# Optimization experiments

Measured on AMD Instinct MI355X. Metric: run time of the kernel, lower is better.

## Reference

```python
import jax, jax.numpy as jnp
import numpy as np

B, S, D, F, E = 8, 2048, 1024, 4096, 5

def setup_inputs() -> dict:
    key = jax.random.key(0)
    ks = jax.random.split(key, 9)
    sc = 0.02
    return {
        "hidden_states": jax.random.normal(ks[0], (B, S, D), jnp.float32),
        "type_label": jax.random.randint(ks[1], (B,), 0, E, jnp.int32),
        "wi": jax.random.normal(ks[2], (E, D, F), jnp.float32) * sc,   # routed experts wi
        "wo": jax.random.normal(ks[3], (E, F, D), jnp.float32) * sc,   # routed experts wo
        "swi": jax.random.normal(ks[4], (2, D, F), jnp.float32) * sc,  # shared experts wi
        "swo": jax.random.normal(ks[5], (2, F, D), jnp.float32) * sc,  # shared experts wo
        "g1": jax.random.normal(ks[6], (3 * D, D), jnp.float32) * sc,  # gate layer 1
        "g2": jax.random.normal(ks[7], (D, 3), jnp.float32) * sc,      # gate layer 2
    }

def _dense(x, wi_, wo_):
    # T5DenseActDense with relu act, dropout=0 (eval)
    return jax.nn.relu(x @ wi_) @ wo_

def reference(hidden_states, type_label, wi, wo, swi, swo, g1, g2):
    x = hidden_states
    s0 = _dense(x, swi[0], swo[0])  # [B,S,D] shared expert 0
    s1 = _dense(x, swi[1], swo[1])  # [B,S,D] shared expert 1
    # per-sample routed expert: gather weights by label, batched GEMM
    wi_sel = wi[type_label]         # [B,D,F]
    wo_sel = wo[type_label]         # [B,F,D]
    h = jax.nn.relu(jnp.einsum('bsd,bdf->bsf', x, wi_sel))
    eo = jnp.einsum('bsf,bfd->bsd', h, wo_sel)  # [B,S,D]
    # gate on token 0 of each stream, all gates share parameters
    gate_in = jnp.concatenate([eo[:, 0], s0[:, 0], s1[:, 0]], axis=-1)  # [B,3D]
    w = jax.nn.softmax(jax.nn.relu(gate_in @ g1) @ g2, axis=-1)         # [B,3]
    w = w[:, :, None, None]
    return eo * w[:, 0] + s0 * w[:, 1] + s1 * w[:, 2]
```

## Files before the change

kernel.cpp:

```cpp
#include <hip/hip_runtime.h>
#include <hip/hip_bf16.h>
#include <cstdint>

#define B_ 8
#define S_ 2048
#define D_ 1024
#define F_ 4096
#define E_ 5

typedef __attribute__((ext_vector_type(4))) int      i32x4;
typedef __attribute__((ext_vector_type(4))) float    f32x4;
typedef __attribute__((ext_vector_type(4))) uint16_t u16x4;
typedef __attribute__((ext_vector_type(8))) uint16_t u16x8;

__device__ __forceinline__ float b2f(uint16_t u){
  union { uint32_t i; float f; } v; v.i = ((uint32_t)u) << 16; return v.f;
}
__device__ __forceinline__ uint16_t f2b(float f){
  union { float f; uint32_t i; } v; v.f = f;
  uint32_t x = v.i;
  uint32_t r = (x + 0x7FFFu + ((x >> 16) & 1u)) >> 16;
  return (uint16_t)r;
}
__device__ __forceinline__ void gload16B(const uint16_t* g, uint16_t* l){
  __builtin_amdgcn_global_load_lds(
      (const __attribute__((address_space(1))) void*)g,
      (__attribute__((address_space(3))) void*)l, 16, 0, 0);
}

__global__ __launch_bounds__(256) void cvt_bf16(
    const float* __restrict__ src, uint16_t* __restrict__ dst, long n)
{
  long i = ((long)blockIdx.x * 256 + threadIdx.x) * 8;
  const long stride = (long)gridDim.x * 256 * 8;
  for (; i + 8 <= n; i += stride){
    f32x4 a = *(const f32x4*)(src + i);
    f32x4 b = *(const f32x4*)(src + i + 4);
    u16x8 r;
#pragma unroll
    for (int k = 0; k < 4; ++k){ r[k] = f2b(a[k]); r[4 + k] = f2b(b[k]); }
    *(u16x8*)(dst + i) = r;
  }
}

__global__ __launch_bounds__(256) void transpose64(
    const float* __restrict__ src, uint16_t* __restrict__ dst, int R, int C)
{
  __shared__ uint16_t t[64][68];
  const size_t base = (size_t)blockIdx.z * R * C;
  const int r0 = blockIdx.x * 64, c0 = blockIdx.y * 64;
  const int tr = threadIdx.x >> 4;
  const int tc = (threadIdx.x & 15) * 4;
#pragma unroll
  for (int i = 0; i < 4; ++i){
    const int row = tr + i * 16;
    f32x4 v = *(const f32x4*)(src + base + (size_t)(r0 + row) * C + (c0 + tc));
    t[row][tc + 0] = f2b(v[0]); t[row][tc + 1] = f2b(v[1]);
    t[row][tc + 2] = f2b(v[2]); t[row][tc + 3] = f2b(v[3]);
  }
  __syncthreads();
#pragma unroll
  for (int i = 0; i < 4; ++i){
    const int orow = tr + i * 16;
    u16x4 v;
    v[0] = t[tc + 0][orow]; v[1] = t[tc + 1][orow];
    v[2] = t[tc + 2][orow]; v[3] = t[tc + 3][orow];
    *(u16x4*)(dst + base + (size_t)(c0 + orow) * R + (r0 + tc)) = v;
  }
}

__global__ __launch_bounds__(256) void transpose_f32(
    const float* __restrict__ src, float* __restrict__ dst, int R, int C)
{
  __shared__ float t[64][65];
  const int r0 = blockIdx.x * 64, c0 = blockIdx.y * 64;
  const int tr = threadIdx.x >> 4;
  const int tc = (threadIdx.x & 15) * 4;
#pragma unroll
  for (int i = 0; i < 4; ++i){
    const int row = tr + i * 16;
    f32x4 v = *(const f32x4*)(src + (size_t)(r0 + row) * C + (c0 + tc));
    t[row][tc + 0] = v[0]; t[row][tc + 1] = v[1];
    t[row][tc + 2] = v[2]; t[row][tc + 3] = v[3];
  }
  __syncthreads();
#pragma unroll
  for (int i = 0; i < 4; ++i){
    const int orow = tr + i * 16;
    f32x4 v;
    v[0] = t[tc + 0][orow]; v[1] = t[tc + 1][orow];
    v[2] = t[tc + 2][orow]; v[3] = t[tc + 3][orow];
    *(f32x4*)(dst + (size_t)(c0 + orow) * R + (r0 + tc)) = v;
  }
}

__global__ __launch_bounds__(256) void gate_h(
    const uint16_t* __restrict__ xb, const uint16_t* __restrict__ wiT,
    const uint16_t* __restrict__ swiT, const int* __restrict__ label,
    float* __restrict__ hbuf)
{
  const int f = blockIdx.x * 256 + threadIdx.x;
  const int path = blockIdx.y, b = blockIdx.z;
  const uint16_t* wrow = (path == 0)
      ? wiT  + ((size_t)label[b] * F_ + f) * D_
      : swiT + ((size_t)(path - 1) * F_ + f) * D_;
  __shared__ uint16_t xs[D_];
  const uint16_t* xr = xb + (size_t)b * S_ * D_;
  *(u16x4*)(xs + threadIdx.x * 4) = *(const u16x4*)(xr + threadIdx.x * 4);
  __syncthreads();
  float acc = 0.f;
  for (int d = 0; d < D_; d += 8){
    u16x8 w = *(const u16x8*)(wrow + d);
    u16x8 xv = *(const u16x8*)(xs + d);
#pragma unroll
    for (int k = 0; k < 8; ++k) acc += b2f(xv[k]) * b2f(w[k]);
  }
  hbuf[(size_t)(b * 3 + path) * F_ + f] = fmaxf(acc, 0.f);
}

__global__ __launch_bounds__(256) void gate_row(
    const uint16_t* __restrict__ woT, const uint16_t* __restrict__ swoT,
    const int* __restrict__ label, const float* __restrict__ hbuf,
    float* __restrict__ gin)
{
  const int d = blockIdx.x * 256 + threadIdx.x;
  const int path = blockIdx.y, b = blockIdx.z;
  const uint16_t* wrow = (path == 0)
      ? woT  + ((size_t)label[b] * D_ + d) * F_
      : swoT + ((size_t)(path - 1) * D_ + d) * F_;
  __shared__ float hs[F_];
  const float* hb = hbuf + (size_t)(b * 3 + path) * F_;
  for (int i = threadIdx.x; i < F_; i += 256) hs[i] = hb[i];
  __syncthreads();
  float acc = 0.f;
  for (int f = 0; f < F_; f += 8){
    u16x8 w = *(const u16x8*)(wrow + f);
    f32x4 h0 = *(const f32x4*)(hs + f);
    f32x4 h1 = *(const f32x4*)(hs + f + 4);
    acc += h0[0]*b2f(w[0]) + h0[1]*b2f(w[1]) + h0[2]*b2f(w[2]) + h0[3]*b2f(w[3])
         + h1[0]*b2f(w[4]) + h1[1]*b2f(w[5]) + h1[2]*b2f(w[6]) + h1[3]*b2f(w[7]);
  }
  gin[(size_t)(b * 3 + path) * D_ + d] = acc;
}

__global__ __launch_bounds__(256) void gate_w1(
    const float* __restrict__ gin, const float* __restrict__ g1T,
    float* __restrict__ ts)
{
  const int j = blockIdx.x * 256 + threadIdx.x;
  const int b = blockIdx.y;
  __shared__ float gs[3 * D_];
  const float* g = gin + (size_t)b * 3 * D_;
  for (int i = threadIdx.x; i < 3 * D_; i += 256) gs[i] = g[i];
  __syncthreads();
  const float* grow = g1T + (size_t)j * (3 * D_);
  float acc = 0.f;
  for (int i = 0; i < 3 * D_; i += 4){
    f32x4 w = *(const f32x4*)(grow + i);
    f32x4 gv = *(const f32x4*)(gs + i);
    acc += gv[0]*w[0] + gv[1]*w[1] + gv[2]*w[2] + gv[3]*w[3];
  }
  ts[(size_t)b * D_ + j] = fmaxf(acc, 0.f);
}

__global__ __launch_bounds__(256) void gate_w2(
    const float* __restrict__ ts, const float* __restrict__ g2,
    float* __restrict__ wgate)
{
  const int b = blockIdx.x;
  __shared__ float p0[256], p1[256], p2[256];
  const float* t = ts + (size_t)b * D_;
  float s0 = 0.f, s1 = 0.f, s2 = 0.f;
  const int j0 = threadIdx.x * 4;
#pragma unroll
  for (int jj = 0; jj < 4; ++jj){
    const float tv = t[j0 + jj];
    s0 += tv * g2[(j0 + jj) * 3 + 0];
    s1 += tv * g2[(j0 + jj) * 3 + 1];
    s2 += tv * g2[(j0 + jj) * 3 + 2];
  }
  p0[threadIdx.x] = s0; p1[threadIdx.x] = s1; p2[threadIdx.x] = s2;
  __syncthreads();
  for (int st = 128; st > 0; st >>= 1){
    if (threadIdx.x < st){
      p0[threadIdx.x] += p0[threadIdx.x + st];
      p1[threadIdx.x] += p1[threadIdx.x + st];
      p2[threadIdx.x] += p2[threadIdx.x + st];
    }
    __syncthreads();
  }
  if (threadIdx.x == 0){
    const float a = p0[0], c = p1[0], d = p2[0];
    const float m = fmaxf(a, fmaxf(c, d));
    const float e0 = expf(a - m), e1 = expf(c - m), e2 = expf(d - m);
    const float inv = 1.f / (e0 + e1 + e2);
    wgate[b * 3 + 0] = e0 * inv;
    wgate[b * 3 + 1] = e1 * inv;
    wgate[b * 3 + 2] = e2 * inv;
  }
}

template<int MODE>
__global__ __launch_bounds__(256) void gemm_bt(
    const uint16_t* __restrict__ Abase, size_t a_stride, int lda, int K,
    const uint16_t* __restrict__ Wexp, const uint16_t* __restrict__ Wsh,
    int path, int b0, const int* __restrict__ label,
    const float* __restrict__ wgate,
    void* __restrict__ Obase_, size_t o_stride, int ldo)
{
  __shared__ uint16_t As[128 * 64];
  __shared__ uint16_t Bs[128 * 64];

  const int z  = blockIdx.z;
  const int b  = b0 + z;
  const int m0 = blockIdx.x * 128;
  const int n0 = blockIdx.y * 128;

  const uint16_t* A = Abase + (size_t)z * a_stride;
  const size_t wstride = (size_t)D_ * F_;
  const uint16_t* BT = (path == 0) ? Wexp + (size_t)label[b] * wstride
                                   : Wsh  + (size_t)(path - 1) * wstride;

  const int tid  = threadIdx.x;
  const int wave = tid >> 6;
  const int lane = tid & 63;

  const uint16_t* gA = A  + (size_t)(m0 + wave * 8 + (lane >> 3)) * lda + (lane & 7) * 8;
  const uint16_t* gB = BT + (size_t)(n0 + wave * 8 + (lane >> 3)) * K   + (lane & 7) * 8;
  uint16_t* lA = As + wave * 512;
  uint16_t* lB = Bs + wave * 512;

  f32x4 acc[4][4];
#pragma unroll
  for (int i = 0; i < 4; ++i)
#pragma unroll
    for (int j = 0; j < 4; ++j) acc[i][j] = (f32x4)0.0f;

  const uint16_t* pa = As + ((wave >> 1) * 64 + (lane & 15)) * 64 + (lane >> 4) * 8;
  const uint16_t* pb = Bs + ((wave &  1) * 64 + (lane & 15)) * 64 + (lane >> 4) * 8;

  const int KT = K >> 6;
  for (int kt = 0; kt < KT; ++kt){
    __syncthreads();
#pragma unroll
    for (int q = 0; q < 4; ++q){
      gload16B(gA + (size_t)q * 32 * lda, lA + q * 2048);
      gload16B(gB + (size_t)q * 32 * K,   lB + q * 2048);
    }
    gA += 64; gB += 64;
    __syncthreads();
#pragma unroll
    for (int ks = 0; ks < 2; ++ks){
      i32x4 af[4], bf[4];
#pragma unroll
      for (int i = 0; i < 4; ++i) af[i] = *(const i32x4*)(pa + i * 1024 + ks * 32);
#pragma unroll
      for (int j = 0; j < 4; ++j) bf[j] = *(const i32x4*)(pb + j * 1024 + ks * 32);
#pragma unroll
      for (int i = 0; i < 4; ++i)
#pragma unroll
        for (int j = 0; j < 4; ++j)
          asm("v_mfma_f32_16x16x32_bf16 %0, %1, %2, %0"
              : "+v"(acc[i][j]) : "v"(af[i]), "v"(bf[j]));
    }
  }

  asm volatile("s_nop 7\n\ts_nop 7" ::);

  const int orow0 = m0 + (wave >> 1) * 64 + (lane >> 4) * 4;
  const int ocol0 = n0 + (wave &  1) * 64 + (lane & 15);

  if constexpr (MODE == 0){
    uint16_t* O = (uint16_t*)Obase_ + (size_t)z * o_stride;
#pragma unroll
    for (int i = 0; i < 4; ++i)
#pragma unroll
      for (int j = 0; j < 4; ++j){
        const int col = ocol0 + j * 16;
#pragma unroll
        for (int r = 0; r < 4; ++r){
          const int row = orow0 + i * 16 + r;
          const float v = acc[i][j][r];
          O[(size_t)row * ldo + col] = f2b(v > 0.f ? v : 0.f);
        }
      }
  } else {
    float* O = (float*)Obase_ + (size_t)z * o_stride;
    const float scale = wgate[b * 3 + path];
#pragma unroll
    for (int i = 0; i < 4; ++i)
#pragma unroll
      for (int j = 0; j < 4; ++j){
        const int col = ocol0 + j * 16;
#pragma unroll
        for (int r = 0; r < 4; ++r){
          const int row = orow0 + i * 16 + r;
          const size_t idx = (size_t)row * ldo + col;
          float v = scale * acc[i][j][r];
          if constexpr (MODE == 2) v += O[idx];
          O[idx] = v;
        }
      }
  }
}

extern "C" void kernel_launch(void* const* d_in, const int* in_sizes, int n_in,
                              void* d_out, int out_size, void* d_ws, size_t ws_size,
                              hipStream_t stream)
{
  (void)in_sizes; (void)n_in; (void)out_size;
  const float* x    = (const float*)d_in[0];
  const int*   label= (const int*)d_in[1];
  const float* wi   = (const float*)d_in[2];
  const float* wo   = (const float*)d_in[3];
  const float* swi  = (const float*)d_in[4];
  const float* swo  = (const float*)d_in[5];
  const float* g1   = (const float*)d_in[6];
  const float* g2   = (const float*)d_in[7];
  float* out = (float*)d_out;

  char* ws = (char*)d_ws;
  float* wgate = (float*)ws;
  float* gin   = (float*)(ws + 256);
  float* hbuf  = (float*)(ws + 98560);
  float* ts    = (float*)(ws + 491776);
  float* g1T   = (float*)(ws + (1u << 20));
  uint16_t* xb = (uint16_t*)(ws + (16u << 20));
  size_t off = (size_t)(16u << 20) + (size_t)B_ * S_ * D_ * 2;
  uint16_t* wiT  = (uint16_t*)(ws + off); off += (size_t)E_ * D_ * F_ * 2;
  uint16_t* swiT = (uint16_t*)(ws + off); off += (size_t)2  * D_ * F_ * 2;
  uint16_t* woT  = (uint16_t*)(ws + off); off += (size_t)E_ * D_ * F_ * 2;
  uint16_t* swoT = (uint16_t*)(ws + off); off += (size_t)2  * D_ * F_ * 2;
  uint16_t* H    = (uint16_t*)(ws + off);
  const size_t hbytes = (size_t)S_ * F_ * 2;
  const size_t hcap = (ws_size > off) ? (ws_size - off) / hbytes : 0;
  const int nb = hcap >= 8 ? 8 : hcap >= 4 ? 4 : hcap >= 2 ? 2 : 1;

  cvt_bf16<<<dim3(2048), 256, 0, stream>>>(x, xb, (long)B_ * S_ * D_);
  transpose64<<<dim3(D_/64, F_/64, E_), 256, 0, stream>>>(wi,  wiT,  D_, F_);
  transpose64<<<dim3(D_/64, F_/64, 2 ), 256, 0, stream>>>(swi, swiT, D_, F_);
  transpose64<<<dim3(F_/64, D_/64, E_), 256, 0, stream>>>(wo,  woT,  F_, D_);
  transpose64<<<dim3(F_/64, D_/64, 2 ), 256, 0, stream>>>(swo, swoT, F_, D_);
  transpose_f32<<<dim3(3*D_/64, D_/64), 256, 0, stream>>>(g1, g1T, 3*D_, D_);

  gate_h  <<<dim3(F_/256, 3, B_), 256, 0, stream>>>(xb, wiT, swiT, label, hbuf);
  gate_row<<<dim3(D_/256, 3, B_), 256, 0, stream>>>(woT, swoT, label, hbuf, gin);
  gate_w1 <<<dim3(D_/256, B_),    256, 0, stream>>>(gin, g1T, ts);
  gate_w2 <<<dim3(B_),            256, 0, stream>>>(ts, g2, wgate);

  const size_t SD = (size_t)S_ * D_;
  const size_t SF = (size_t)S_ * F_;
  for (int path = 0; path < 3; ++path){
    for (int b0 = 0; b0 < B_; b0 += nb){
      const int nbc = (b0 + nb <= B_) ? nb : (B_ - b0);
      gemm_bt<0><<<dim3(S_/128, F_/128, nbc), 256, 0, stream>>>(
          xb + (size_t)b0 * SD, SD, D_, D_, wiT, swiT, path, b0, label,
          (const float*)nullptr, H, SF, F_);
      if (path == 0)
        gemm_bt<1><<<dim3(S_/128, D_/128, nbc), 256, 0, stream>>>(
            H, SF, F_, F_, woT, swoT, path, b0, label, wgate,
            out + (size_t)b0 * SD, SD, D_);
      else
        gemm_bt<2><<<dim3(S_/128, D_/128, nbc), 256, 0, stream>>>(
            H, SF, F_, F_, woT, swoT, path, b0, label, wgate,
            out + (size_t)b0 * SD, SD, D_);
    }
  }
}
```

Measured before the change: 1.272 ms.

## Double-buffer LDS tiles to prefetch next K-tile during MFMA compute

```diff
diff --git a/kernel.cpp b/kernel.cpp
--- a/kernel.cpp
+++ b/kernel.cpp
@@ -208,8 +208,8 @@
     const float* __restrict__ wgate,
     void* __restrict__ Obase_, size_t o_stride, int ldo)
 {
-  __shared__ uint16_t As[128 * 64];
-  __shared__ uint16_t Bs[128 * 64];
+  __shared__ uint16_t As[2][128 * 64];
+  __shared__ uint16_t Bs[2][128 * 64];
 
   const int z  = blockIdx.z;
   const int b  = b0 + z;
@@ -227,8 +227,6 @@
 
   const uint16_t* gA = A  + (size_t)(m0 + wave * 8 + (lane >> 3)) * lda + (lane & 7) * 8;
   const uint16_t* gB = BT + (size_t)(n0 + wave * 8 + (lane >> 3)) * K   + (lane & 7) * 8;
-  uint16_t* lA = As + wave * 512;
-  uint16_t* lB = Bs + wave * 512;
 
   f32x4 acc[4][4];
 #pragma unroll
@@ -236,19 +234,33 @@
 #pragma unroll
     for (int j = 0; j < 4; ++j) acc[i][j] = (f32x4)0.0f;
 
-  const uint16_t* pa = As + ((wave >> 1) * 64 + (lane & 15)) * 64 + (lane >> 4) * 8;
-  const uint16_t* pb = Bs + ((wave &  1) * 64 + (lane & 15)) * 64 + (lane >> 4) * 8;
+  const int fa = ((wave >> 1) * 64 + (lane & 15)) * 64 + (lane >> 4) * 8;
+  const int fb = ((wave &  1) * 64 + (lane & 15)) * 64 + (lane >> 4) * 8;
+
+#define STAGE_T(sel, kt) do {                                              \
+    const uint16_t* _ga = gA + (size_t)(kt) * 64;                          \
+    const uint16_t* _gb = gB + (size_t)(kt) * 64;                          \
+    uint16_t* _la = &As[sel][wave * 512];                                  \
+    uint16_t* _lb = &Bs[sel][wave * 512];                                  \
+    _Pragma("unroll")                                                      \
+    for (int q = 0; q < 4; ++q){                                           \
+      gload16B(_ga + (size_t)q * 32 * lda, _la + q * 2048);                \
+      gload16B(_gb + (size_t)q * 32 * K,   _lb + q * 2048);                \
+    }                                                                      \
+  } while (0)
 
   const int KT = K >> 6;
+
+  STAGE_T(0, 0);
+  __syncthreads();
+
   for (int kt = 0; kt < KT; ++kt){
-    __syncthreads();
-#pragma unroll
-    for (int q = 0; q < 4; ++q){
-      gload16B(gA + (size_t)q * 32 * lda, lA + q * 2048);
-      gload16B(gB + (size_t)q * 32 * K,   lB + q * 2048);
-    }
-    gA += 64; gB += 64;
-    __syncthreads();
+    const int sel = kt & 1;
+    if (kt + 1 < KT) STAGE_T(sel ^ 1, kt + 1);
+
+    const uint16_t* pa = &As[sel][fa];
+    const uint16_t* pb = &Bs[sel][fb];
+    __builtin_amdgcn_s_setprio(1);
 #pragma unroll
     for (int ks = 0; ks < 2; ++ks){
       i32x4 af[4], bf[4];
@@ -263,7 +275,11 @@
           asm("v_mfma_f32_16x16x32_bf16 %0, %1, %2, %0"
               : "+v"(acc[i][j]) : "v"(af[i]), "v"(bf[j]));
     }
-  }
+    __builtin_amdgcn_s_setprio(0);
+
+    if (kt + 1 < KT) __syncthreads();
+  }
+#undef STAGE_T
 
   asm volatile("s_nop 7\n\ts_nop 7" ::);
 
```

Result: slower. 1.600 ms (+25.9%).

## Fuse three expert paths into one concatenated-K second GEMM with gate-scaled H

Applied to the files above, without the earlier changes.

```diff
diff --git a/kernel.cpp b/kernel.cpp
--- a/kernel.cpp
+++ b/kernel.cpp
@@ -200,6 +200,55 @@
   }
 }
 
+#define KLOOP_BODY(gA, gB, LDA, KK)                                         \
+  {                                                                         \
+    const int KT = (KK) >> 6;                                               \
+    for (int kt = 0; kt < KT; ++kt){                                        \
+      __syncthreads();                        \
+      _Pragma("unroll")                                                     \
+      for (int q = 0; q < 4; ++q){                                          \
+        gload16B((gA) + (size_t)q * 32 * (LDA), lA + q * 2048);             \
+        gload16B((gB) + (size_t)q * 32 * (KK), lB + q * 2048);              \
+      }                                                                     \
+      (gA) += 64; (gB) += 64;                                               \
+      __syncthreads();                        \
+      _Pragma("unroll")                                                     \
+      for (int ks = 0; ks < 2; ++ks){                                       \
+        i32x4 af[4], bf[4];                                                 \
+        _Pragma("unroll")                                                   \
+        for (int i = 0; i < 4; ++i)                                         \
+          af[i] = *(const i32x4*)(pa + i * 1024 + ks * 32);                 \
+        _Pragma("unroll")                                                   \
+        for (int j = 0; j < 4; ++j)                                         \
+          bf[j] = *(const i32x4*)(pb + j * 1024 + ks * 32);                 \
+        _Pragma("unroll")                                                   \
+        for (int i = 0; i < 4; ++i)                                         \
+          _Pragma("unroll")                                                 \
+          for (int j = 0; j < 4; ++j)                                       \
+            asm("v_mfma_f32_16x16x32_bf16 %0, %1, %2, %0"                   \
+                : "+v"(acc[i][j]) : "v"(af[i]), "v"(bf[j]));                \
+      }                                                                     \
+    }                                                                       \
+  }
+
+#define GEMM_PREAMBLE                                                       \
+  __shared__ uint16_t As[128 * 64];                                         \
+  __shared__ uint16_t Bs[128 * 64];                                         \
+  const int tid  = threadIdx.x;                                             \
+  const int wave = tid >> 6;                                                \
+  const int lane = tid & 63;                                                \
+  uint16_t* lA = As + wave * 512;                                           \
+  uint16_t* lB = Bs + wave * 512;                                           \
+  f32x4 acc[4][4];                                                          \
+  _Pragma("unroll")                                                         \
+  for (int i = 0; i < 4; ++i)                                               \
+    _Pragma("unroll")                                                       \
+    for (int j = 0; j < 4; ++j) acc[i][j] = (f32x4)0.0f;                    \
+  const uint16_t* pa = As + ((wave >> 1) * 64 + (lane & 15)) * 64           \
+                          + (lane >> 4) * 8;                                \
+  const uint16_t* pb = Bs + ((wave &  1) * 64 + (lane & 15)) * 64           \
+                          + (lane >> 4) * 8;
+
 template<int MODE>
 __global__ __launch_bounds__(256) void gemm_bt(
     const uint16_t* __restrict__ Abase, size_t a_stride, int lda, int K,
@@ -208,9 +257,7 @@
     const float* __restrict__ wgate,
     void* __restrict__ Obase_, size_t o_stride, int ldo)
 {
-  __shared__ uint16_t As[128 * 64];
-  __shared__ uint16_t Bs[128 * 64];
-
+  GEMM_PREAMBLE
   const int z  = blockIdx.z;
   const int b  = b0 + z;
   const int m0 = blockIdx.x * 128;
@@ -221,52 +268,12 @@
   const uint16_t* BT = (path == 0) ? Wexp + (size_t)label[b] * wstride
                                    : Wsh  + (size_t)(path - 1) * wstride;
 
-  const int tid  = threadIdx.x;
-  const int wave = tid >> 6;
-  const int lane = tid & 63;
-
   const uint16_t* gA = A  + (size_t)(m0 + wave * 8 + (lane >> 3)) * lda + (lane & 7) * 8;
   const uint16_t* gB = BT + (size_t)(n0 + wave * 8 + (lane >> 3)) * K   + (lane & 7) * 8;
-  uint16_t* lA = As + wave * 512;
-  uint16_t* lB = Bs + wave * 512;
-
-  f32x4 acc[4][4];
-#pragma unroll
-  for (int i = 0; i < 4; ++i)
-#pragma unroll
-    for (int j = 0; j < 4; ++j) acc[i][j] = (f32x4)0.0f;
-
-  const uint16_t* pa = As + ((wave >> 1) * 64 + (lane & 15)) * 64 + (lane >> 4) * 8;
-  const uint16_t* pb = Bs + ((wave &  1) * 64 + (lane & 15)) * 64 + (lane >> 4) * 8;
-
-  const int KT = K >> 6;
-  for (int kt = 0; kt < KT; ++kt){
-    __syncthreads();
-#pragma unroll
-    for (int q = 0; q < 4; ++q){
-      gload16B(gA + (size_t)q * 32 * lda, lA + q * 2048);
-      gload16B(gB + (size_t)q * 32 * K,   lB + q * 2048);
-    }
-    gA += 64; gB += 64;
-    __syncthreads();
-#pragma unroll
-    for (int ks = 0; ks < 2; ++ks){
-      i32x4 af[4], bf[4];
-#pragma unroll
-      for (int i = 0; i < 4; ++i) af[i] = *(const i32x4*)(pa + i * 1024 + ks * 32);
-#pragma unroll
-      for (int j = 0; j < 4; ++j) bf[j] = *(const i32x4*)(pb + j * 1024 + ks * 32);
-#pragma unroll
-      for (int i = 0; i < 4; ++i)
-#pragma unroll
-        for (int j = 0; j < 4; ++j)
-          asm("v_mfma_f32_16x16x32_bf16 %0, %1, %2, %0"
-              : "+v"(acc[i][j]) : "v"(af[i]), "v"(bf[j]));
-    }
-  }
+
+  KLOOP_BODY(gA, gB, lda, K)
 
   asm volatile("s_nop 7\n\ts_nop 7" ::);
-
   const int orow0 = m0 + (wave >> 1) * 64 + (lane >> 4) * 4;
   const int ocol0 = n0 + (wave &  1) * 64 + (lane & 15);
 
@@ -302,6 +309,83 @@
         }
       }
   }
+}
+
+__global__ __launch_bounds__(256) void gemm1_all(
+    const uint16_t* __restrict__ xb, const uint16_t* __restrict__ wiT,
+    const uint16_t* __restrict__ swiT, const int* __restrict__ label,
+    const float* __restrict__ wgate, uint16_t* __restrict__ H)
+{
+  GEMM_PREAMBLE
+  const int path = blockIdx.z >> 3;
+  const int b    = blockIdx.z & 7;
+  const int m0 = blockIdx.x * 128;
+  const int n0 = blockIdx.y * 128;
+
+  const uint16_t* A = xb + (size_t)b * S_ * D_;
+  const size_t wstride = (size_t)D_ * F_;
+  const uint16_t* BT = (path == 0) ? wiT  + (size_t)label[b] * wstride
+                                   : swiT + (size_t)(path - 1) * wstride;
+
+  const uint16_t* gA = A  + (size_t)(m0 + wave * 8 + (lane >> 3)) * D_ + (lane & 7) * 8;
+  const uint16_t* gB = BT + (size_t)(n0 + wave * 8 + (lane >> 3)) * D_ + (lane & 7) * 8;
+
+  KLOOP_BODY(gA, gB, D_, D_)
+
+  asm volatile("s_nop 7\n\ts_nop 7" ::);
+  const int orow0 = m0 + (wave >> 1) * 64 + (lane >> 4) * 4;
+  const int ocol0 = n0 + (wave &  1) * 64 + (lane & 15);
+  const float scale = wgate[b * 3 + path];
+  uint16_t* O = H + ((size_t)path * B_ + b) * S_ * F_;
+#pragma unroll
+  for (int i = 0; i < 4; ++i)
+#pragma unroll
+    for (int j = 0; j < 4; ++j){
+      const int col = ocol0 + j * 16;
+#pragma unroll
+      for (int r = 0; r < 4; ++r){
+        const int row = orow0 + i * 16 + r;
+        const float v = acc[i][j][r];
+        O[(size_t)row * F_ + col] = f2b(v > 0.f ? scale * v : 0.f);
+      }
+    }
+}
+
+__global__ __launch_bounds__(256) void gemm2_fused(
+    const uint16_t* __restrict__ H, const uint16_t* __restrict__ woT,
+    const uint16_t* __restrict__ swoT, const int* __restrict__ label,
+    float* __restrict__ out)
+{
+  GEMM_PREAMBLE
+  const int b  = blockIdx.z;
+  const int m0 = blockIdx.x * 128;
+  const int n0 = blockIdx.y * 128;
+  const size_t wstride = (size_t)D_ * F_;
+
+  for (int seg = 0; seg < 3; ++seg){
+    const uint16_t* A  = H + ((size_t)seg * B_ + b) * S_ * F_;
+    const uint16_t* BT = (seg == 0) ? woT  + (size_t)label[b] * wstride
+                                    : swoT + (size_t)(seg - 1) * wstride;
+    const uint16_t* gA = A  + (size_t)(m0 + wave * 8 + (lane >> 3)) * F_ + (lane & 7) * 8;
+    const uint16_t* gB = BT + (size_t)(n0 + wave * 8 + (lane >> 3)) * F_ + (lane & 7) * 8;
+    KLOOP_BODY(gA, gB, F_, F_)
+  }
+
+  asm volatile("s_nop 7\n\ts_nop 7" ::);
+  const int orow0 = m0 + (wave >> 1) * 64 + (lane >> 4) * 4;
+  const int ocol0 = n0 + (wave &  1) * 64 + (lane & 15);
+  float* O = out + (size_t)b * S_ * D_;
+#pragma unroll
+  for (int i = 0; i < 4; ++i)
+#pragma unroll
+    for (int j = 0; j < 4; ++j){
+      const int col = ocol0 + j * 16;
+#pragma unroll
+      for (int r = 0; r < 4; ++r){
+        const int row = orow0 + i * 16 + r;
+        O[(size_t)row * D_ + col] = acc[i][j][r];
+      }
+    }
 }
 
 extern "C" void kernel_launch(void* const* d_in, const int* in_sizes, int n_in,
@@ -334,6 +418,7 @@
   uint16_t* H    = (uint16_t*)(ws + off);
   const size_t hbytes = (size_t)S_ * F_ * 2;
   const size_t hcap = (ws_size > off) ? (ws_size - off) / hbytes : 0;
+  const bool fused = hcap >= (size_t)3 * B_;
   const int nb = hcap >= 8 ? 8 : hcap >= 4 ? 4 : hcap >= 2 ? 2 : 1;
 
   cvt_bf16<<<dim3(2048), 256, 0, stream>>>(x, xb, (long)B_ * S_ * D_);
@@ -350,20 +435,28 @@
 
   const size_t SD = (size_t)S_ * D_;
   const size_t SF = (size_t)S_ * F_;
-  for (int path = 0; path < 3; ++path){
-    for (int b0 = 0; b0 < B_; b0 += nb){
-      const int nbc = (b0 + nb <= B_) ? nb : (B_ - b0);
-      gemm_bt<0><<<dim3(S_/128, F_/128, nbc), 256, 0, stream>>>(
-          xb + (size_t)b0 * SD, SD, D_, D_, wiT, swiT, path, b0, label,
-          (const float*)nullptr, H, SF, F_);
-      if (path == 0)
-        gemm_bt<1><<<dim3(S_/128, D_/128, nbc), 256, 0, stream>>>(
-            H, SF, F_, F_, woT, swoT, path, b0, label, wgate,
-            out + (size_t)b0 * SD, SD, D_);
-      else
-        gemm_bt<2><<<dim3(S_/128, D_/128, nbc), 256, 0, stream>>>(
-            H, SF, F_, F_, woT, swoT, path, b0, label, wgate,
-            out + (size_t)b0 * SD, SD, D_);
+
+  if (fused){
+    gemm1_all  <<<dim3(S_/128, F_/128, 3 * B_), 256, 0, stream>>>(
+        xb, wiT, swiT, label, wgate, H);
+    gemm2_fused<<<dim3(S_/128, D_/128, B_),     256, 0, stream>>>(
+        H, woT, swoT, label, out);
+  } else {
+    for (int path = 0; path < 3; ++path){
+      for (int b0 = 0; b0 < B_; b0 += nb){
+        const int nbc = (b0 + nb <= B_) ? nb : (B_ - b0);
+        gemm_bt<0><<<dim3(S_/128, F_/128, nbc), 256, 0, stream>>>(
+            xb + (size_t)b0 * SD, SD, D_, D_, wiT, swiT, path, b0, label,
+            (const float*)nullptr, H, SF, F_);
+        if (path == 0)
+          gemm_bt<1><<<dim3(S_/128, D_/128, nbc), 256, 0, stream>>>(
+              H, SF, F_, F_, woT, swoT, path, b0, label, wgate,
+              out + (size_t)b0 * SD, SD, D_);
+        else
+          gemm_bt<2><<<dim3(S_/128, D_/128, nbc), 256, 0, stream>>>(
+              H, SF, F_, F_, woT, swoT, path, b0, label, wgate,
+              out + (size_t)b0 * SD, SD, D_);
+      }
     }
   }
 }
```

Result: no change. 1.274 ms (+0.2%).
